# Performance work log

Measured on AMD Instinct MI355X. Metric: run time of the kernel, lower is better.

Reference implementation:

```python
import jax, jax.numpy as jnp
import numpy as np

KER = 8  # patch size used by unfold/fold
EPS = 1e-5


def _gelu(x):
    return jax.nn.gelu(x, approximate=False)  # torch nn.GELU default (exact erf)


def _conv(x, w, b):
    # x: [B,C,H,W], w: [O,I,kh,kw]
    y = jax.lax.conv_general_dilated(x, w, (1, 1), 'SAME',
                                     dimension_numbers=('NCHW', 'OIHW', 'NCHW'))
    return y + b[None, :, None, None]


def _unfold_t(x):
    # F.unfold(k=8, s=8).transpose(1,2): [B,C,H,W] -> [B, L, C*k*k]
    B, C, H, W = x.shape
    Hp, Wp = H // KER, W // KER
    x = x.reshape(B, C, Hp, KER, Wp, KER)
    x = x.transpose(0, 2, 4, 1, 3, 5)  # [B,Hp,Wp,C,k,k]
    return x.reshape(B, Hp * Wp, C * KER * KER)


def _fold(y, H, W):
    # inverse of unfold (non-overlapping): [B,L,C*k*k] -> [B,C,H,W]
    B, L, D = y.shape
    Hp, Wp = H // KER, W // KER
    C = D // (KER * KER)
    y = y.reshape(B, Hp, Wp, C, KER, KER).transpose(0, 3, 1, 4, 2, 5)
    return y.reshape(B, C, H, W)


def _bn1d(x, gamma, beta):
    # BatchNorm1d (training-mode batch stats) on [B, C, L]: stats over (B, L)
    m = x.mean(axis=(0, 2), keepdims=True)
    v = x.var(axis=(0, 2), keepdims=True)  # biased variance, matches torch fwd
    return (x - m) * jax.lax.rsqrt(v + EPS) * gamma[None, :, None] + beta[None, :, None]


def setup_inputs() -> dict:
    key = jax.random.key(0)
    ks = jax.random.split(key, 12)
    B, C, H, W = 4, 64, 256, 256
    dq = KER * KER * C  # 4096

    def n(k, shape, scale=0.02):
        return jax.random.normal(k, shape, jnp.float32) * scale

    return {
        'feat': jax.random.normal(ks[0], (B, C, H, W), jnp.float32),
        'w_enc': n(ks[1], (C, C, 3, 3)), 'b_enc': jnp.zeros((C,), jnp.float32),
        'w_kc': n(ks[2], (C, C, 3, 3)), 'b_kc': jnp.zeros((C,), jnp.float32),
        'w_vc': n(ks[3], (C, C, 3, 3)), 'b_vc': jnp.zeros((C,), jnp.float32),
        'wq': n(ks[4], (1024, dq)), 'bq': jnp.zeros((1024,), jnp.float32),
        'wk': n(ks[5], (1024, dq)), 'bk': jnp.zeros((1024,), jnp.float32),
        'gq': jnp.ones((1024,), jnp.float32), 'betaq': jnp.zeros((1024,), jnp.float32),
        'gk': jnp.ones((1024,), jnp.float32), 'betak': jnp.zeros((1024,), jnp.float32),
        'w_f1': n(ks[6], (4 * C, C, 1, 1)), 'b_f1': jnp.zeros((4 * C,), jnp.float32),
        'w_f2': n(ks[7], (C, 4 * C, 1, 1)), 'b_f2': jnp.zeros((C,), jnp.float32),
    }


def reference(feat, w_enc, b_enc, w_kc, b_kc, w_vc, b_vc, wq, bq, wk, bk,
              gq, betaq, gk, betak, w_f1, b_f1, w_f2, b_f2):
    H, W = feat.shape[-2:]
    refer = _gelu(_conv(feat, w_enc, b_enc))
    feat_k = _gelu(_conv(feat, w_kc, b_kc))
    feat_v = _gelu(_conv(feat, w_vc, b_vc))

    q_un = _unfold_t(refer)   # [B,L,4096]
    k_un = _unfold_t(feat_k)
    v_un = _unfold_t(feat_v)

    # Linear -> BN1d over 1024 channels (transpose dance as in the torch code)
    qp = _bn1d((q_un @ wq.T + bq).transpose(0, 2, 1), gq, betaq).transpose(0, 2, 1)  # [B,L,1024]
    kp = _bn1d((k_un @ wk.T + bk).transpose(0, 2, 1), gk, betak).transpose(0, 2, 1)  # [B,L,1024]

    scale = jnp.sqrt(jnp.asarray(qp.shape[2], qp.dtype))
    scores = jnp.einsum('bld,bmd->blm', qp, kp) / scale  # [B,L,L]
    attn = jax.nn.softmax(scores, axis=2)
    out = jnp.einsum('blm,bmd->bld', attn, v_un)  # [B,L,4096]

    out = _fold(out, H, W)  # [B,C,H,W]
    ff = _gelu(_conv(out, w_f1, b_f1))
    ff = _gelu(_conv(ff, w_f2, b_f2))
    return ff + feat
```

## Files before the change

kernel.cpp:

```cpp
#include <hip/hip_runtime.h>
#include <hip/hip_bf16.h>

typedef unsigned short u16;
typedef __attribute__((ext_vector_type(8))) short short8v;
typedef __attribute__((ext_vector_type(8))) unsigned short u16x8;
typedef __attribute__((ext_vector_type(4))) float f32x4;

#define HWPIX 65536

__device__ __forceinline__ float bfbits2f(u16 u) {
  return __uint_as_float(((unsigned)u) << 16);
}
__device__ __forceinline__ float4 ld4bf(const u16* p) {
  ushort4 u = *(const ushort4*)(const void*)p;
  return make_float4(bfbits2f(u.x), bfbits2f(u.y), bfbits2f(u.z), bfbits2f(u.w));
}
__device__ __forceinline__ u16 f2bf(float f) {
  union { __hip_bfloat16 h; u16 u; } c;
  c.h = __float2bfloat16(f);
  return c.u;
}
__device__ __forceinline__ float gelu_f(float x) {
  return 0.5f * x * (1.0f + erff(x * 0.70710678118654752440f));
}
__device__ __forceinline__ u16x8 bn8(u16x8 v, const float* __restrict__ sc,
                                     const float* __restrict__ sh, int kk) {
  float4 s0 = *(const float4*)&sc[kk], s1 = *(const float4*)&sc[kk + 4];
  float4 t0 = *(const float4*)&sh[kk], t1 = *(const float4*)&sh[kk + 4];
  u16x8 r;
  r[0] = f2bf(bfbits2f(v[0]) * s0.x + t0.x); r[1] = f2bf(bfbits2f(v[1]) * s0.y + t0.y);
  r[2] = f2bf(bfbits2f(v[2]) * s0.z + t0.z); r[3] = f2bf(bfbits2f(v[3]) * s0.w + t0.w);
  r[4] = f2bf(bfbits2f(v[4]) * s1.x + t1.x); r[5] = f2bf(bfbits2f(v[5]) * s1.y + t1.y);
  r[6] = f2bf(bfbits2f(v[6]) * s1.z + t1.z); r[7] = f2bf(bfbits2f(v[7]) * s1.w + t1.w);
  return r;
}

__launch_bounds__(256)
__global__ void nhwc_k(const float* __restrict__ x, u16* __restrict__ y) {
  __shared__ float tile[64][65];
  const int t = threadIdx.x;
  const int xs = blockIdx.x << 6, yy = blockIdx.y, b = blockIdx.z;
#pragma unroll
  for (int it = 0; it < 4; ++it) {
    const int idx = t + it * 256;
    const int c = idx >> 4, seg = (idx & 15) << 2;
    float4 v = *(const float4*)&x[(((size_t)(b * 64 + c)) << 16) + yy * 256 + xs + seg];
    tile[c][seg] = v.x; tile[c][seg + 1] = v.y; tile[c][seg + 2] = v.z; tile[c][seg + 3] = v.w;
  }
  __syncthreads();
#pragma unroll
  for (int it = 0; it < 4; ++it) {
    const int idx = t + it * 256;
    const int cs = (idx & 15) << 2, px = idx >> 4;
    ushort4 r;
    r.x = f2bf(tile[cs + 0][px]); r.y = f2bf(tile[cs + 1][px]);
    r.z = f2bf(tile[cs + 2][px]); r.w = f2bf(tile[cs + 3][px]);
    *(ushort4*)&y[(((size_t)((b * 256 + yy) * 256 + xs + px)) << 6) + cs] = r;
  }
}

__launch_bounds__(256)
__global__ void wcvt2_k(const float* __restrict__ s0, u16* __restrict__ d0,
                        const float* __restrict__ s1, u16* __restrict__ d1) {
  const float* src = blockIdx.y ? s1 : s0;
  u16* dst = blockIdx.y ? d1 : d0;
  const int i = (blockIdx.x * 256 + threadIdx.x) << 2;
  float4 v = *(const float4*)&src[i];
  ushort4 r;
  r.x = f2bf(v.x); r.y = f2bf(v.y); r.z = f2bf(v.z); r.w = f2bf(v.w);
  *(ushort4*)&dst[i] = r;
}

__launch_bounds__(256)
__global__ void wprep_k(const float* __restrict__ w0, const float* __restrict__ w1,
                        const float* __restrict__ w2, const float* __restrict__ b0,
                        const float* __restrict__ b1, const float* __restrict__ b2,
                        const float* __restrict__ wf1, const float* __restrict__ wf2,
                        u16* __restrict__ wT, float* __restrict__ bias192,
                        u16* __restrict__ wf1b, u16* __restrict__ wf2b) {
  const int t = threadIdx.x;
  const int bx = blockIdx.x;
  if (bx >= 497) {
    const int e = (bx - 497) * 256 + t;
    wf2b[e] = f2bf(wf2[e]);
    return;
  }
  if (bx >= 433) {
    const int e = (bx - 433) * 256 + t;
    wf1b[e] = f2bf(wf1[e]);
    return;
  }
  if (bx == 432) {
    if (t < 192) {
      const float* bp = (t < 64) ? b0 : (t < 128) ? b1 : b2;
      bias192[t] = bp[t & 63];
    }
    return;
  }
  const int e = bx * 256 + t;
  const int pos = e / 12288, rem = e % 12288;
  const int n = rem >> 6, ic = rem & 63;
  const int conv = n >> 6, oc = n & 63;
  const float* wp = (conv == 0) ? w0 : (conv == 1) ? w1 : w2;
  wT[e] = f2bf(wp[(oc * 64 + ic) * 9 + pos]);
}

__launch_bounds__(256)
__global__ void convmfma_k(const u16* __restrict__ featb, const u16* __restrict__ wT,
                           const float* __restrict__ bias192, u16* __restrict__ qun,
                           u16* __restrict__ kun, u16* __restrict__ vT) {
  __shared__ u16 As[2][128 * 40];
  __shared__ u16 Bs[2][192 * 40];
  const int tid = threadIdx.x;
  const int lin = blockIdx.x;
  const int virt = (lin & 7) * 256 + (lin >> 3);
  const int b = virt >> 9, yy = (virt >> 1) & 255, x0 = (virt & 1) << 7;
  const int lane = tid & 63, w = tid >> 6;
  const int wm = w >> 1, wn = w & 1;

  const int arow = tid >> 1, acs = (tid & 1) << 4;
  const int brow0 = tid >> 2, bseg0 = (tid & 3) << 3;

  u16x8 pA0, pA1, pB0, pB1, pB2;

  auto issue = [&](int s) {
    const int pos = s >> 1, half = (s & 1) << 5;
    const int dy = pos / 3, dx = pos % 3;
    const int yp = yy + dy - 1;
    const int xp = x0 + arow + dx - 1;
    if ((unsigned)yp < 256u && (unsigned)xp < 256u) {
      const u16* src = featb + (((size_t)((b * 256 + yp) * 256 + xp)) << 6) + half + acs;
      pA0 = *(const u16x8*)src;
      pA1 = *(const u16x8*)(src + 8);
    } else {
      pA0 = u16x8{}; pA1 = u16x8{};
    }
    const u16* wb = wT + (size_t)pos * 12288 + half;
    pB0 = *(const u16x8*)&wb[(brow0 + 0) * 64 + bseg0];
    pB1 = *(const u16x8*)&wb[(brow0 + 64) * 64 + bseg0];
    pB2 = *(const u16x8*)&wb[(brow0 + 128) * 64 + bseg0];
  };
  auto commit = [&](int buf) {
    *(u16x8*)&As[buf][arow * 40 + acs] = pA0;
    *(u16x8*)&As[buf][arow * 40 + acs + 8] = pA1;
    *(u16x8*)&Bs[buf][(brow0 + 0) * 40 + bseg0] = pB0;
    *(u16x8*)&Bs[buf][(brow0 + 64) * 40 + bseg0] = pB1;
    *(u16x8*)&Bs[buf][(brow0 + 128) * 40 + bseg0] = pB2;
  };

  f32x4 acc[4][6] = {};
  issue(0);
  commit(0);
  __syncthreads();

  int cur = 0;
  const int kc = (lane >> 4) << 3;
  const int afr = wm * 64 + (lane & 15);
  const int bfr0 = wn * 96 + (lane & 15);
  for (int s = 0; s < 18; ++s) {
    if (s + 1 < 18) issue(s + 1);
    const u16* Asb = As[cur];
    const u16* Bsb = Bs[cur];
    short8v a[4], bf[6];
#pragma unroll
    for (int f = 0; f < 4; ++f) a[f] = *(const short8v*)&Asb[(afr + f * 16) * 40 + kc];
#pragma unroll
    for (int f = 0; f < 6; ++f) bf[f] = *(const short8v*)&Bsb[(bfr0 + f * 16) * 40 + kc];
#pragma unroll
    for (int i = 0; i < 4; ++i)
#pragma unroll
      for (int j = 0; j < 6; ++j)
        acc[i][j] = __builtin_amdgcn_mfma_f32_16x16x32_bf16(a[i], bf[j], acc[i][j], 0, 0, 0);
    if (s + 1 < 18) commit(cur ^ 1);
    __syncthreads();
    cur ^= 1;
  }

  const int py = yy >> 3, ky = yy & 7;
  const int rp0 = wm * 64 + ((lane >> 4) << 2);
#pragma unroll
  for (int j = 0; j < 6; ++j) {
    const int colb = wn * 96 + j * 16;
    const int conv = colb >> 6;
    const int oc = (colb & 63) + (lane & 15);
    const float bj = bias192[colb + (lane & 15)];
#pragma unroll
    for (int i = 0; i < 4; ++i) {
      const int rp = rp0 + i * 16;
      const int xg = x0 + rp;
      const int px = xg >> 3, kx0 = xg & 7;
      float v0 = gelu_f(acc[i][j][0] + bj);
      float v1 = gelu_f(acc[i][j][1] + bj);
      float v2 = gelu_f(acc[i][j][2] + bj);
      float v3 = gelu_f(acc[i][j][3] + bj);
      const int d0 = (oc << 6) + (ky << 3) + kx0;
      if (conv < 2) {
        u16* dst = conv ? kun : qun;
        const size_t addr = (((size_t)((b << 10) + py * 32 + px)) << 12) + d0;
        ushort4 r4;
        r4.x = f2bf(v0); r4.y = f2bf(v1); r4.z = f2bf(v2); r4.w = f2bf(v3);
        *(ushort4*)&dst[addr] = r4;
      } else {
        const int m = py * 32 + px;
        const size_t base = (((size_t)(b * 4096 + d0)) << 10) + m;
        vT[base] = f2bf(v0);
        vT[base + 1024] = f2bf(v1);
        vT[base + 2048] = f2bf(v2);
        vT[base + 3072] = f2bf(v3);
      }
    }
  }
}

__launch_bounds__(256)
__global__ void bnpart_k(const u16* __restrict__ q, const u16* __restrict__ k,
                         float2* __restrict__ part) {
  const u16* x = blockIdx.y ? k : q;
  const int b = blockIdx.x, t = threadIdx.x;
  const int c = t << 2;
  float s0 = 0.f, s1 = 0.f, s2 = 0.f, s3 = 0.f;
  float q0 = 0.f, q1 = 0.f, q2 = 0.f, q3 = 0.f;
  const u16* base = x + ((size_t)b << 15) + c;
#pragma unroll 4
  for (int r = 0; r < 32; ++r) {
    float4 v = ld4bf(base + (r << 10));
    s0 += v.x; q0 += v.x * v.x;
    s1 += v.y; q1 += v.y * v.y;
    s2 += v.z; q2 += v.z * v.z;
    s3 += v.w; q3 += v.w * v.w;
  }
  float2* dst = part + (((size_t)(blockIdx.y * 128 + b)) << 10) + c;
  dst[0] = make_float2(s0, q0);
  dst[1] = make_float2(s1, q1);
  dst[2] = make_float2(s2, q2);
  dst[3] = make_float2(s3, q3);
}
__launch_bounds__(256)
__global__ void bnfin_k(const float2* __restrict__ part, const float* __restrict__ gq,
                        const float* __restrict__ betaq, const float* __restrict__ gk,
                        const float* __restrict__ betak, float* __restrict__ scq,
                        float* __restrict__ shq, float* __restrict__ sck,
                        float* __restrict__ shk) {
  const int n = blockIdx.x * 256 + threadIdx.x;
  const int y = blockIdx.y;
  const float2* p = part + (((size_t)(y * 128)) << 10) + n;
  float S = 0.f, S2 = 0.f;
  for (int i = 0; i < 128; ++i) {
    float2 v = p[(size_t)i << 10];
    S += v.x; S2 += v.y;
  }
  const float mean = S * (1.0f / 4096.0f);
  const float var = S2 * (1.0f / 4096.0f) - mean * mean;
  const float rstd = rsqrtf(var + 1e-5f);
  const float g = (y ? gk : gq)[n];
  const float be = (y ? betak : betaq)[n];
  const float sc = g * rstd;
  (y ? sck : scq)[n] = sc;
  (y ? shk : shq)[n] = be - mean * sc;
}

__launch_bounds__(256)
__global__ void softmax_k(u16* __restrict__ s) {
  u16* p = s + (size_t)blockIdx.x * 1024;
  const int tid = threadIdx.x;
  float4 v = ld4bf(p + (tid << 2));
  float mx = fmaxf(fmaxf(v.x, v.y), fmaxf(v.z, v.w));
#pragma unroll
  for (int off = 32; off > 0; off >>= 1) mx = fmaxf(mx, __shfl_xor(mx, off));
  __shared__ float red[8];
  if ((tid & 63) == 0) red[tid >> 6] = mx;
  __syncthreads();
  mx = fmaxf(fmaxf(red[0], red[1]), fmaxf(red[2], red[3]));
  float e0 = __expf(v.x - mx), e1 = __expf(v.y - mx), e2 = __expf(v.z - mx), e3 = __expf(v.w - mx);
  float sm = e0 + e1 + e2 + e3;
#pragma unroll
  for (int off = 32; off > 0; off >>= 1) sm += __shfl_xor(sm, off);
  if ((tid & 63) == 0) red[4 + (tid >> 6)] = sm;
  __syncthreads();
  sm = red[4] + red[5] + red[6] + red[7];
  float inv = 1.0f / sm;
  ushort4 r;
  r.x = f2bf(e0 * inv); r.y = f2bf(e1 * inv); r.z = f2bf(e2 * inv); r.w = f2bf(e3 * inv);
  *(ushort4*)&p[tid << 2] = r;
}

template <int MODE>
__launch_bounds__(512)
__global__ void mgemm8_k(const u16* __restrict__ Ap0, const u16* __restrict__ Bp0,
                         const float* __restrict__ sA, const float* __restrict__ hA,
                         const float* __restrict__ sB, const float* __restrict__ hB,
                         const float* __restrict__ bias0, u16* __restrict__ Cp0, int K,
                         const u16* __restrict__ Ap2, const u16* __restrict__ Bp2,
                         const float* __restrict__ bias2, u16* __restrict__ Cp2) {
  constexpr int SD = (MODE == 0) ? 4096 : 1024;
  __shared__ u16 As[2][128 * 72];
  __shared__ u16 Bs[2][128 * 72];
  const int tid = threadIdx.x;

  int bx, by, z;
  if constexpr (MODE == 2) {
    int lin = blockIdx.x + 32 * blockIdx.y + 256 * blockIdx.z;
    int sw = (lin & 7) * 128 + (lin >> 3);
    bx = sw & 31; by = (sw >> 5) & 7; z = sw >> 8;
  } else {
    bx = blockIdx.x; by = blockIdx.y; z = blockIdx.z;
  }
  const u16* Ap = Ap0;
  const u16* Bp = Bp0;
  const float* bias = bias0;
  u16* Cp = Cp0;
  if constexpr (MODE == 0) {
    if (z) { Ap = Ap2; Bp = Bp2; bias = bias2; Cp = Cp2; }
  }
  const int m0 = by * 128, n0 = bx * 128;
  const int lane = tid & 63, w = tid >> 6;
  const int wm = w >> 2, wn = w & 3;

  const int srow = tid >> 3;
  const int scol = (tid & 7) << 3;
  const size_t zoffA = (MODE == 0) ? 0 : ((size_t)z << 10);
  const size_t zoffB = (MODE == 0) ? 0 : (MODE == 1) ? ((size_t)z << 10) : ((size_t)z << 12);
  const u16* A0 = Ap + (zoffA + m0 + srow) * (size_t)SD + scol;
  const u16* A1 = A0 + (size_t)64 * SD;
  const u16* B0 = Bp + (zoffB + n0 + srow) * (size_t)SD + scol;
  const u16* B1 = B0 + (size_t)64 * SD;
  const int l0 = srow * 72 + scol;
  const int l1 = (srow + 64) * 72 + scol;

  const int NT = K >> 6;
  u16x8 pA0 = *(const u16x8*)A0;
  u16x8 pA1 = *(const u16x8*)A1;
  u16x8 pB0 = *(const u16x8*)B0;
  u16x8 pB1 = *(const u16x8*)B1;
  if constexpr (MODE == 1) {
    pA0 = bn8(pA0, sA, hA, scol); pA1 = bn8(pA1, sA, hA, scol);
    pB0 = bn8(pB0, sB, hB, scol); pB1 = bn8(pB1, sB, hB, scol);
  }
  *(u16x8*)&As[0][l0] = pA0; *(u16x8*)&As[0][l1] = pA1;
  *(u16x8*)&Bs[0][l0] = pB0; *(u16x8*)&Bs[0][l1] = pB1;
  __syncthreads();

  f32x4 acc[4][2] = {};
  int cur = 0;
  for (int t = 0; t < NT; ++t) {
    const int kn = (t + 1) << 6;
    if (t + 1 < NT) {
      pA0 = *(const u16x8*)(A0 + kn);
      pA1 = *(const u16x8*)(A1 + kn);
      pB0 = *(const u16x8*)(B0 + kn);
      pB1 = *(const u16x8*)(B1 + kn);
    }
    const u16* Asb = As[cur];
    const u16* Bsb = Bs[cur];
#pragma unroll
    for (int ks = 0; ks < 2; ++ks) {
      const int kc = ks * 32 + ((lane >> 4) << 3);
      short8v a[4], bfr[2];
#pragma unroll
      for (int f = 0; f < 4; ++f)
        a[f] = *(const short8v*)&Asb[(wm * 64 + (lane & 15) + f * 16) * 72 + kc];
#pragma unroll
      for (int f = 0; f < 2; ++f)
        bfr[f] = *(const short8v*)&Bsb[(wn * 32 + (lane & 15) + f * 16) * 72 + kc];
#pragma unroll
      for (int i = 0; i < 4; ++i)
#pragma unroll
        for (int j = 0; j < 2; ++j)
          acc[i][j] = __builtin_amdgcn_mfma_f32_16x16x32_bf16(a[i], bfr[j], acc[i][j], 0, 0, 0);
    }
    if (t + 1 < NT) {
      if constexpr (MODE == 1) {
        pA0 = bn8(pA0, sA, hA, kn + scol); pA1 = bn8(pA1, sA, hA, kn + scol);
        pB0 = bn8(pB0, sB, hB, kn + scol); pB1 = bn8(pB1, sB, hB, kn + scol);
      }
      *(u16x8*)&As[cur ^ 1][l0] = pA0; *(u16x8*)&As[cur ^ 1][l1] = pA1;
      *(u16x8*)&Bs[cur ^ 1][l0] = pB0; *(u16x8*)&Bs[cur ^ 1][l1] = pB1;
    }
    __syncthreads();
    cur ^= 1;
  }

  const int rowbase = m0 + wm * 64 + ((lane >> 4) << 2);
  const int colbase = n0 + wn * 32 + (lane & 15);
  if constexpr (MODE == 2) {
    const size_t coff = (size_t)(8 + 8 * z) * 524288;
    u16* C = Cp + coff;
#pragma unroll
    for (int j = 0; j < 2; ++j) {
      const int d = colbase + j * 16;
      const int c = d >> 6, ky = (d >> 3) & 7, kx = d & 7;
#pragma unroll
      for (int i = 0; i < 4; ++i)
#pragma unroll
        for (int r = 0; r < 4; ++r) {
          const int l = rowbase + i * 16 + r;
          const int p = (((l >> 5) << 3) + ky) * 256 + ((l & 31) << 3) + kx;
          C[((size_t)p << 6) + c] = f2bf(acc[i][j][r]);
        }
    }
  } else {
#pragma unroll
    for (int j = 0; j < 2; ++j) {
      const int col = colbase + j * 16;
      float bj = 0.f;
      if constexpr (MODE == 0) bj = bias[col];
#pragma unroll
      for (int i = 0; i < 4; ++i)
#pragma unroll
        for (int r = 0; r < 4; ++r) {
          const size_t row = (MODE == 1 ? ((size_t)z << 10) : 0) + rowbase + i * 16 + r;
          float v = (MODE == 0) ? (acc[i][j][r] + bj) : (acc[i][j][r] * 0.03125f);
          Cp[row * 1024 + col] = f2bf(v);
        }
    }
  }
}

__launch_bounds__(512)
__global__ void ffn_k(const u16* __restrict__ fold, const u16* __restrict__ w1b,
                      const u16* __restrict__ w2b, const float* __restrict__ b1,
                      const float* __restrict__ b2, const float* __restrict__ feat,
                      float* __restrict__ out) {
  extern __shared__ u16 sh[];
  u16* Ash = sh;
  u16* W1s = sh + 9216;
  u16* mids = sh;
  const int t = threadIdx.x;
  const int px0 = blockIdx.x << 7;
  const int z = blockIdx.y;
  const u16* fz = fold + ((size_t)z << 22);

  {
    const int row = t >> 2, cs = (t & 3) << 4;
    const u16* src = fz + (((size_t)(px0 + row)) << 6) + cs;
    *(u16x8*)&Ash[row * 72 + cs] = *(const u16x8*)src;
    *(u16x8*)&Ash[row * 72 + cs + 8] = *(const u16x8*)(src + 8);
  }
  {
    const int row = t >> 1, cs = (t & 1) << 5;
    const u16* src = w1b + (((size_t)row) << 6) + cs;
    *(u16x8*)&W1s[row * 72 + cs] = *(const u16x8*)src;
    *(u16x8*)&W1s[row * 72 + cs + 8] = *(const u16x8*)(src + 8);
    *(u16x8*)&W1s[row * 72 + cs + 16] = *(const u16x8*)(src + 16);
    *(u16x8*)&W1s[row * 72 + cs + 24] = *(const u16x8*)(src + 24);
  }
  __syncthreads();

  const int lane = t & 63, w = t >> 6;
  const int kc = (lane >> 4) << 3;
  const int mrow = w * 16 + (lane & 15);
  f32x4 acc1[16] = {};
  short8v a0 = *(const short8v*)&Ash[mrow * 72 + kc];
  short8v a1 = *(const short8v*)&Ash[mrow * 72 + 32 + kc];
#pragma unroll
  for (int n = 0; n < 16; ++n) {
    const int br = n * 16 + (lane & 15);
    short8v b0 = *(const short8v*)&W1s[br * 72 + kc];
    short8v bv = *(const short8v*)&W1s[br * 72 + 32 + kc];
    acc1[n] = __builtin_amdgcn_mfma_f32_16x16x32_bf16(a0, b0, acc1[n], 0, 0, 0);
    acc1[n] = __builtin_amdgcn_mfma_f32_16x16x32_bf16(a1, bv, acc1[n], 0, 0, 0);
  }
  __syncthreads();

  const int mrow0 = w * 16 + ((lane >> 4) << 2);
#pragma unroll
  for (int n = 0; n < 16; ++n) {
    const int col = n * 16 + (lane & 15);
    const float bj = b1[col];
#pragma unroll
    for (int r = 0; r < 4; ++r)
      mids[(mrow0 + r) * 264 + col] = f2bf(gelu_f(acc1[n][r] + bj));
  }
  __syncthreads();

  f32x4 acc2[4] = {};
#pragma unroll
  for (int ks = 0; ks < 8; ++ks) {
    short8v a2 = *(const short8v*)&mids[(w * 16 + (lane & 15)) * 264 + ks * 32 + kc];
#pragma unroll
    for (int n = 0; n < 4; ++n) {
      short8v bv = *(const short8v*)(const void*)&w2b[(size_t)(n * 16 + (lane & 15)) * 256 + ks * 32 + kc];
      acc2[n] = __builtin_amdgcn_mfma_f32_16x16x32_bf16(a2, bv, acc2[n], 0, 0, 0);
    }
  }
#pragma unroll
  for (int n = 0; n < 4; ++n) {
    const int oc = n * 16 + (lane & 15);
    const float bn = b2[oc];
    const int px = px0 + mrow0;
    const size_t base = (((size_t)(z * 64 + oc)) << 16) + px;
    float4 f = *(const float4*)&feat[base];
    float4 rv;
    rv.x = gelu_f(acc2[n][0] + bn) + f.x;
    rv.y = gelu_f(acc2[n][1] + bn) + f.y;
    rv.z = gelu_f(acc2[n][2] + bn) + f.z;
    rv.w = gelu_f(acc2[n][3] + bn) + f.w;
    *(float4*)&out[base] = rv;
  }
}

extern "C" void kernel_launch(void* const* d_in, const int* in_sizes, int n_in,
                              void* d_out, int out_size, void* d_ws, size_t ws_size,
                              hipStream_t stream) {
  const float* feat  = (const float*)d_in[0];
  const float* w_enc = (const float*)d_in[1];
  const float* b_enc = (const float*)d_in[2];
  const float* w_kc  = (const float*)d_in[3];
  const float* b_kc  = (const float*)d_in[4];
  const float* w_vc  = (const float*)d_in[5];
  const float* b_vc  = (const float*)d_in[6];
  const float* wq    = (const float*)d_in[7];
  const float* bq    = (const float*)d_in[8];
  const float* wk    = (const float*)d_in[9];
  const float* bk    = (const float*)d_in[10];
  const float* gq    = (const float*)d_in[11];
  const float* betaq = (const float*)d_in[12];
  const float* gk    = (const float*)d_in[13];
  const float* betak = (const float*)d_in[14];
  const float* w_f1  = (const float*)d_in[15];
  const float* b_f1  = (const float*)d_in[16];
  const float* w_f2  = (const float*)d_in[17];
  const float* b_f2  = (const float*)d_in[18];

  char* ws = (char*)d_ws;
  const size_t MB = (size_t)1 << 20;
  u16*   qun    = (u16*)(ws);
  u16*   kun    = (u16*)(ws + 32 * MB);
  u16*   qlin   = (u16*)(ws + 64 * MB);
  u16*   klin   = (u16*)(ws + 40 * MB);
  u16*   wqb    = (u16*)(ws + 72 * MB);
  u16*   wT     = (u16*)(ws + 80 * MB);
  float* bias192= (float*)(ws + 80 * MB + 224 * 1024);
  float* scaleq = (float*)(ws + 80 * MB + 232 * 1024);
  float* shiftq = scaleq + 1024;
  float* scalek = shiftq + 1024;
  float* shiftk = scalek + 1024;
  u16*   wf1b   = (u16*)(ws + 80 * MB + 512 * 1024);
  u16*   wf2b   = (u16*)(ws + 80 * MB + 576 * 1024);
  float2* bnpart = (float2*)(ws + 81 * MB);
  u16*   scores = (u16*)(ws);
  u16*   featb  = (u16*)d_out;
  u16*   vT     = (u16*)((char*)d_out + 32 * MB);
  u16*   wkb    = (u16*)d_out;

  const dim3 blk(256);
  const dim3 blk8(512);
  nhwc_k<<<dim3(4, 256, 4), blk, 0, stream>>>(feat, featb);
  wprep_k<<<561, blk, 0, stream>>>(w_enc, w_kc, w_vc, b_enc, b_kc, b_vc,
                                   w_f1, w_f2, wT, bias192, wf1b, wf2b);
  convmfma_k<<<2048, blk, 0, stream>>>(featb, wT, bias192, qun, kun, vT);
  wcvt2_k<<<dim3(4096, 2), blk, 0, stream>>>(wq, wqb, wk, wkb);
  mgemm8_k<0><<<dim3(8, 32, 2), blk8, 0, stream>>>(qun, wqb, nullptr, nullptr, nullptr, nullptr,
                                                   bq, qlin, 4096, kun, wkb, bk, klin);
  bnpart_k<<<dim3(128, 2), blk, 0, stream>>>(qlin, klin, bnpart);
  bnfin_k<<<dim3(4, 2), blk, 0, stream>>>(bnpart, gq, betaq, gk, betak, scaleq, shiftq, scalek, shiftk);
  mgemm8_k<1><<<dim3(8, 8, 4), blk8, 0, stream>>>(qlin, klin, scaleq, shiftq, scalek, shiftk,
                                                  nullptr, scores, 1024, nullptr, nullptr, nullptr, nullptr);
  softmax_k<<<4096, blk, 0, stream>>>(scores);
  mgemm8_k<2><<<dim3(32, 8, 4), blk8, 0, stream>>>(scores, vT, nullptr, nullptr, nullptr, nullptr,
                                                   nullptr, (u16*)ws, 1024, nullptr, nullptr, nullptr, nullptr);
  ffn_k<<<dim3(512, 4), blk8, 67584, stream>>>((u16*)(ws + 8 * MB), wf1b, wf2b, b_f1, b_f2, feat, (float*)d_out);
  (void)in_sizes; (void)n_in; (void)out_size; (void)ws_size;
}
```

Before: 493.9 us.

## Use tanh-approx GELU and single-buffer LDS in the fused conv kernel

Replaces the exact erf GELU with a tanh approximation built from a fast exp and a hardware reciprocal, which cuts the transcendental cost in every GELU epilogue. It also removes the register-staged double buffering in the 3x3 conv MFMA kernel. Each step now loads global data straight into a single LDS buffer with two barriers per step, which halves LDS use and lowers register pressure but no longer overlaps global loads with MFMA work. The tanh GELU departs from the reference's exact erf formulation and adds small numerical error.

```diff
diff --git a/kernel.cpp b/kernel.cpp
--- a/kernel.cpp
+++ b/kernel.cpp
@@ -21,7 +21,10 @@
   return c.u;
 }
 __device__ __forceinline__ float gelu_f(float x) {
-  return 0.5f * x * (1.0f + erff(x * 0.70710678118654752440f));
+  float z = 0.79788456f * x * (1.0f + 0.044715f * x * x);
+  float e = __expf(2.0f * z);
+  float th = 1.0f - 2.0f * __builtin_amdgcn_rcpf(e + 1.0f);
+  return 0.5f * x * (1.0f + th);
 }
 __device__ __forceinline__ u16x8 bn8(u16x8 v, const float* __restrict__ sc,
                                      const float* __restrict__ sh, int kk) {
@@ -109,8 +112,8 @@
 __global__ void convmfma_k(const u16* __restrict__ featb, const u16* __restrict__ wT,
                            const float* __restrict__ bias192, u16* __restrict__ qun,
                            u16* __restrict__ kun, u16* __restrict__ vT) {
-  __shared__ u16 As[2][128 * 40];
-  __shared__ u16 Bs[2][192 * 40];
+  __shared__ u16 As[128 * 40];
+  __shared__ u16 Bs[192 * 40];
   const int tid = threadIdx.x;
   const int lin = blockIdx.x;
   const int virt = (lin & 7) * 256 + (lin >> 3);
@@ -121,59 +124,44 @@
   const int arow = tid >> 1, acs = (tid & 1) << 4;
   const int brow0 = tid >> 2, bseg0 = (tid & 3) << 3;
 
-  u16x8 pA0, pA1, pB0, pB1, pB2;
-
-  auto issue = [&](int s) {
-    const int pos = s >> 1, half = (s & 1) << 5;
-    const int dy = pos / 3, dx = pos % 3;
-    const int yp = yy + dy - 1;
-    const int xp = x0 + arow + dx - 1;
-    if ((unsigned)yp < 256u && (unsigned)xp < 256u) {
-      const u16* src = featb + (((size_t)((b * 256 + yp) * 256 + xp)) << 6) + half + acs;
-      pA0 = *(const u16x8*)src;
-      pA1 = *(const u16x8*)(src + 8);
-    } else {
-      pA0 = u16x8{}; pA1 = u16x8{};
-    }
-    const u16* wb = wT + (size_t)pos * 12288 + half;
-    pB0 = *(const u16x8*)&wb[(brow0 + 0) * 64 + bseg0];
-    pB1 = *(const u16x8*)&wb[(brow0 + 64) * 64 + bseg0];
-    pB2 = *(const u16x8*)&wb[(brow0 + 128) * 64 + bseg0];
-  };
-  auto commit = [&](int buf) {
-    *(u16x8*)&As[buf][arow * 40 + acs] = pA0;
-    *(u16x8*)&As[buf][arow * 40 + acs + 8] = pA1;
-    *(u16x8*)&Bs[buf][(brow0 + 0) * 40 + bseg0] = pB0;
-    *(u16x8*)&Bs[buf][(brow0 + 64) * 40 + bseg0] = pB1;
-    *(u16x8*)&Bs[buf][(brow0 + 128) * 40 + bseg0] = pB2;
-  };
-
   f32x4 acc[4][6] = {};
-  issue(0);
-  commit(0);
-  __syncthreads();
-
-  int cur = 0;
   const int kc = (lane >> 4) << 3;
   const int afr = wm * 64 + (lane & 15);
   const int bfr0 = wn * 96 + (lane & 15);
+
   for (int s = 0; s < 18; ++s) {
-    if (s + 1 < 18) issue(s + 1);
-    const u16* Asb = As[cur];
-    const u16* Bsb = Bs[cur];
+    const int pos = s >> 1, half = (s & 1) << 5;
+    const int dy = pos / 3, dx = pos % 3;
+    {
+      const int yp = yy + dy - 1;
+      const int xp = x0 + arow + dx - 1;
+      u16x8 pA0{}, pA1{};
+      if ((unsigned)yp < 256u && (unsigned)xp < 256u) {
+        const u16* src = featb + (((size_t)((b * 256 + yp) * 256 + xp)) << 6) + half + acs;
+        pA0 = *(const u16x8*)src;
+        pA1 = *(const u16x8*)(src + 8);
+      }
+      *(u16x8*)&As[arow * 40 + acs] = pA0;
+      *(u16x8*)&As[arow * 40 + acs + 8] = pA1;
+    }
+    {
+      const u16* wb = wT + (size_t)pos * 12288 + half;
+      *(u16x8*)&Bs[(brow0 + 0) * 40 + bseg0] = *(const u16x8*)&wb[(brow0 + 0) * 64 + bseg0];
+      *(u16x8*)&Bs[(brow0 + 64) * 40 + bseg0] = *(const u16x8*)&wb[(brow0 + 64) * 64 + bseg0];
+      *(u16x8*)&Bs[(brow0 + 128) * 40 + bseg0] = *(const u16x8*)&wb[(brow0 + 128) * 64 + bseg0];
+    }
+    __syncthreads();
     short8v a[4], bf[6];
 #pragma unroll
-    for (int f = 0; f < 4; ++f) a[f] = *(const short8v*)&Asb[(afr + f * 16) * 40 + kc];
-#pragma unroll
-    for (int f = 0; f < 6; ++f) bf[f] = *(const short8v*)&Bsb[(bfr0 + f * 16) * 40 + kc];
+    for (int f = 0; f < 4; ++f) a[f] = *(const short8v*)&As[(afr + f * 16) * 40 + kc];
+#pragma unroll
+    for (int f = 0; f < 6; ++f) bf[f] = *(const short8v*)&Bs[(bfr0 + f * 16) * 40 + kc];
 #pragma unroll
     for (int i = 0; i < 4; ++i)
 #pragma unroll
       for (int j = 0; j < 6; ++j)
         acc[i][j] = __builtin_amdgcn_mfma_f32_16x16x32_bf16(a[i], bf[j], acc[i][j], 0, 0, 0);
-    if (s + 1 < 18) commit(cur ^ 1);
     __syncthreads();
-    cur ^= 1;
   }
 
   const int py = yy >> 3, ky = yy & 7;
```

Result: no change. 491.5 us (-0.5%).
